# Kernel tuning notes

Hardware: AMD Instinct MI355X
Metric: run time of the kernel (lower is better)

Reference implementation:

```python
import jax, jax.numpy as jnp
import numpy as np

N_EMBD = 512
Q_N_EMBD = 512
N_HEAD = 8
EPS = 1e-5


def _layernorm(x, w, b):
    mu = jnp.mean(x, axis=-1, keepdims=True)
    var = jnp.mean(jnp.square(x - mu), axis=-1, keepdims=True)
    return (x - mu) * jax.lax.rsqrt(var + EPS) * w + b


def setup_inputs() -> dict:
    key = jax.random.key(0)
    ks = jax.random.split(key, 16)
    B, C, H, W = 8, N_EMBD, 32, 32
    s = 1.0 / np.sqrt(N_EMBD)
    inp = {
        "q": jax.random.normal(ks[0], (B, Q_N_EMBD, H, W), jnp.float32),
        "kv": jax.random.normal(ks[1], (B, C, H, W), jnp.float32),
        "ln_kv_w": jnp.ones((N_EMBD,), jnp.float32),
        "ln_kv_b": jnp.zeros((N_EMBD,), jnp.float32),
        "ln_q_w": jnp.ones((Q_N_EMBD,), jnp.float32),
        "ln_q_b": jnp.zeros((Q_N_EMBD,), jnp.float32),
        "Wk": jax.random.normal(ks[2], (N_EMBD, N_EMBD), jnp.float32) * s,
        "bk": jnp.zeros((N_EMBD,), jnp.float32),
        "Wq": jax.random.normal(ks[3], (Q_N_EMBD, N_EMBD), jnp.float32) * s,
        "bq": jnp.zeros((N_EMBD,), jnp.float32),
        "Wv": jax.random.normal(ks[4], (N_EMBD, N_EMBD), jnp.float32) * s,
        "bv": jnp.zeros((N_EMBD,), jnp.float32),
        "Wp": jax.random.normal(ks[5], (N_EMBD, N_EMBD), jnp.float32) * s,
        "bp": jnp.zeros((N_EMBD,), jnp.float32),
    }
    return inp


def reference(q, kv, ln_kv_w, ln_kv_b, ln_q_w, ln_q_b,
              Wk, bk, Wq, bq, Wv, bv, Wp, bp):
    B, C, H, W = kv.shape
    c_q = q.shape[1]
    T = H * W
    hd = C // N_HEAD  # head dim

    # [B, C, H, W] -> [B, T, C] tokens
    kv_t = kv.reshape(B, C, T).transpose(0, 2, 1)
    q_t = q.reshape(B, c_q, T).transpose(0, 2, 1)

    kv_n = _layernorm(kv_t, ln_kv_w, ln_kv_b)
    q_n = _layernorm(q_t, ln_q_w, ln_q_b)

    # projections, split heads: [B, T, C] -> [B, H, T, hd]
    def heads(x):
        return x.reshape(B, T, N_HEAD, hd).transpose(0, 2, 1, 3)

    k = heads(kv_n @ Wk + bk)
    qh = heads(q_n @ Wq + bq)
    v = heads(kv_n @ Wv + bv)

    att = jnp.einsum('bhqd,bhkd->bhqk', qh, k) * (1.0 / np.sqrt(hd))
    att = jax.nn.softmax(att, axis=-1)
    y = jnp.einsum('bhqk,bhkd->bhqd', att, v)
    y = y.transpose(0, 2, 1, 3).reshape(B, T, C)
    y = y @ Wp + bp

    x = kv_t + y  # residual on (pre-LN) kv tokens
    return x.transpose(0, 2, 1).reshape(B, C, H, W)
```

## Files before the change

kernel.cpp:

```cpp
#include <hip/hip_runtime.h>
#include <stdint.h>

#define DI static __device__ __forceinline__

typedef __attribute__((ext_vector_type(8))) short bh8;
typedef __attribute__((ext_vector_type(4))) float f4;

DI short f2bf(float f) {
  unsigned u = __float_as_uint(f);
  u += 0x7fffu + ((u >> 16) & 1u);
  return (short)(u >> 16);
}

DI unsigned pkbf(float a, float b) {
  unsigned ua = __float_as_uint(a) + 0x8000u;
  unsigned ub = __float_as_uint(b) + 0x8000u;
  return __builtin_amdgcn_perm(ub, ua, 0x07060302u);
}

DI unsigned char f2fp8(float f) {
  return (unsigned char)(__builtin_amdgcn_cvt_pk_fp8_f32(f, f, 0, false) & 0xff);
}

DI void gll16(const void* g, void* l) {
  __builtin_amdgcn_global_load_lds(
      (const __attribute__((address_space(1))) unsigned int*)g,
      (__attribute__((address_space(3))) unsigned int*)l, 16, 0, 0);
}

DI f4 mfma16(bh8 a, bh8 b, f4 c) {
  return __builtin_amdgcn_mfma_f32_16x16x32_bf16(a, b, c, 0, 0, 0);
}

DI f4 mfma8(long a, long b, f4 c) {
  return __builtin_amdgcn_mfma_f32_16x16x32_fp8_fp8(a, b, c, 0, 0, 0);
}

DI bh8 ld8(const short* p) { return *(const bh8*)p; }

__global__ __launch_bounds__(256) void prep_k(
    const float* __restrict__ kv, const float* __restrict__ qi,
    const float* __restrict__ kw, const float* __restrict__ kbv,
    const float* __restrict__ qw, const float* __restrict__ qbv,
    const float* __restrict__ Wk, const float* __restrict__ Wq,
    const float* __restrict__ Wv, const float* __restrict__ Wp,
    short* __restrict__ kvn, short* __restrict__ qn,
    short* __restrict__ Wt)
{
  __shared__ char sm[16 * 516 * 4 + 128];
  int role = blockIdx.y;
  int bx = blockIdx.x;
  int tid = threadIdx.x;

  if (role < 4) {
    if (bx >= 256) return;
    float (*ts)[33] = (float(*)[33])sm;
    const float* w = (role == 0) ? Wk : (role == 1) ? Wq : (role == 2) ? Wv : Wp;
    short* o = Wt + ((size_t)role << 18);
    int c0 = (bx & 15) << 5, r0 = (bx >> 4) << 5;
    int tx = tid & 31, ty = tid >> 5;
#pragma unroll
    for (int k = 0; k < 32; k += 8)
      ts[ty + k][tx] = w[((size_t)(r0 + ty + k) << 9) + c0 + tx];
    __syncthreads();
#pragma unroll
    for (int k = 0; k < 32; k += 8)
      o[((size_t)(c0 + ty + k) << 9) + r0 + tx] = f2bf(ts[tx][ty + k]);
    return;
  }

  float (*xs)[516] = (float(*)[516])sm;
  float* smean = (float*)(sm + 16 * 516 * 4);
  float* srstd = smean + 16;
  int which = role - 4;
  const float* x = which ? qi : kv;
  const float* w = which ? qw : kw;
  const float* bb = which ? qbv : kbv;
  short* o = which ? qn : kvn;
  int b = bx >> 6;
  int t0 = (bx & 63) << 4;
  const float* xb = x + ((size_t)b << 19) + (size_t)t0;
#pragma unroll
  for (int k = 0; k < 8; k++) {
    int idx = (k << 8) + tid;
    int c = idx >> 2, tt = (idx & 3) << 2;
    float4 v = *(const float4*)(xb + ((size_t)c << 10) + tt);
    xs[tt + 0][c] = v.x; xs[tt + 1][c] = v.y;
    xs[tt + 2][c] = v.z; xs[tt + 3][c] = v.w;
  }
  __syncthreads();
  {
    int t = tid >> 4, cp = tid & 15;
    float s = 0.f, s2 = 0.f;
#pragma unroll
    for (int k = 0; k < 8; k++) {
      float4 v = *(const float4*)&xs[t][(cp << 2) + (k << 6)];
      s  += v.x + v.y + v.z + v.w;
      s2 += v.x * v.x + v.y * v.y + v.z * v.z + v.w * v.w;
    }
#pragma unroll
    for (int m = 1; m < 16; m <<= 1) {
      s  += __shfl_xor(s,  m);
      s2 += __shfl_xor(s2, m);
    }
    if (cp == 0) {
      float mean = s * (1.f / 512.f);
      float var  = s2 * (1.f / 512.f) - mean * mean;
      smean[t] = mean;
      srstd[t] = rsqrtf(var + 1e-5f);
    }
  }
  __syncthreads();
#pragma unroll
  for (int k = 0; k < 8; k++) {
    int idx = (k << 8) + tid;
    int t = idx >> 7, c = (idx & 127) << 2;
    float4 v = *(const float4*)&xs[t][c];
    float4 wv = *(const float4*)(w + c);
    float4 bv4 = *(const float4*)(bb + c);
    float mu = smean[t], rs = srstd[t];
    float r0 = (v.x - mu) * rs * wv.x + bv4.x;
    float r1 = (v.y - mu) * rs * wv.y + bv4.y;
    float r2 = (v.z - mu) * rs * wv.z + bv4.z;
    float r3 = (v.w - mu) * rs * wv.w + bv4.w;
    uint2 pk; pk.x = pkbf(r0, r1); pk.y = pkbf(r2, r3);
    *(uint2*)(o + (((size_t)(b << 10) + t0 + t) << 9) + c) = pk;
  }
}

__global__ __launch_bounds__(256, 3) void gemm_qkv_k(
    const short* __restrict__ kvn, const short* __restrict__ qn,
    const short* __restrict__ Wt,
    const float* __restrict__ bk, const float* __restrict__ bq,
    const float* __restrict__ bv,
    unsigned char* __restrict__ kb8, unsigned char* __restrict__ qb8,
    unsigned char* __restrict__ vb8)
{
  __shared__ short As[128 * 64];
  __shared__ short Bs[128 * 64];
  int z = blockIdx.z;
  const short* A; const short* Bt; const float* bias;
  int m0, n0;
  if (z == 0)      { A = kvn;            Bt = Wt;             bias = bk; }
  else if (z == 1) { A = qn;             Bt = Wt + (1 << 18); bias = bq; }
  else             { A = Wt + (2 << 18); Bt = kvn;            bias = bv; }
  if (z == 2) { m0 = blockIdx.y << 7; n0 = blockIdx.x << 7; }
  else        { m0 = blockIdx.x << 7; n0 = blockIdx.y << 7; }
  int tid = threadIdx.x;
  int lane = tid & 63, wid = tid >> 6;
  int r = lane & 15, g = lane >> 4;
  int wrow = (wid >> 1) << 6, wcol = (wid & 1) << 6;
  f4 acc[4][4];
#pragma unroll
  for (int i = 0; i < 4; i++)
#pragma unroll
    for (int j = 0; j < 4; j++) {
      acc[i][j][0] = 0.f; acc[i][j][1] = 0.f;
      acc[i][j][2] = 0.f; acc[i][j][3] = 0.f;
    }
  for (int k0 = 0; k0 < 512; k0 += 64) {
    __syncthreads();
#pragma unroll
    for (int it = 0; it < 4; it++) {
      int n = (it << 8) + tid;
      int row = n >> 3;
      int c = (n & 7) ^ (row & 7);
      gll16(A  + ((size_t)(m0 + row) << 9) + k0 + (c << 3), As + (n << 3));
      gll16(Bt + ((size_t)(n0 + row) << 9) + k0 + (c << 3), Bs + (n << 3));
    }
    __syncthreads();
    bh8 a[2][4], b[2][4];
#pragma unroll
    for (int ks = 0; ks < 2; ks++) {
#pragma unroll
      for (int i = 0; i < 4; i++) {
        int R = wrow + (i << 4) + r;
        a[ks][i] = ld8(As + (R << 6) + ((((ks << 2) + g) ^ (R & 7)) << 3));
      }
#pragma unroll
      for (int j = 0; j < 4; j++) {
        int R = wcol + (j << 4) + r;
        b[ks][j] = ld8(Bs + (R << 6) + ((((ks << 2) + g) ^ (R & 7)) << 3));
      }
    }
#pragma unroll
    for (int ks = 0; ks < 2; ks++)
#pragma unroll
      for (int i = 0; i < 4; i++)
#pragma unroll
        for (int j = 0; j < 4; j++)
          acc[i][j] = mfma16(a[ks][i], b[ks][j], acc[i][j]);
  }
#pragma unroll
  for (int i = 0; i < 4; i++) {
#pragma unroll
    for (int j = 0; j < 4; j++) {
      int mm = m0 + wrow + (i << 4) + (g << 2);
      int nn = n0 + wcol + (j << 4) + r;
      if (z == 0) {
        float bvv = bias[nn];
        int h = nn >> 6, d = nn & 63;
#pragma unroll
        for (int q = 0; q < 4; q++) {
          int m = mm + q;
          int bb = m >> 10, t = m & 1023;
          int c = t & 255;
          int p = ((c & 15) << 4) | (c >> 4);
          size_t base = ((size_t)((bb * 8 + h) * 4 + (t >> 8)) << 14);
          kb8[base + (p << 6) + (((d >> 3) ^ (p & 7)) << 3) + (d & 7)] =
              f2fp8(acc[i][j][q] + bvv);
        }
      } else if (z == 1) {
        float bvv = bias[nn];
        int h = nn >> 6, d = nn & 63;
#pragma unroll
        for (int q = 0; q < 4; q++) {
          int m = mm + q;
          int bb = m >> 10, t = m & 1023;
          qb8[((((size_t)(bb * 8 + h)) << 10) + t) * 64 + d] =
              f2fp8(acc[i][j][q] + bvv);
        }
      } else {
        int bb = nn >> 10, t = nn & 1023;
        int tb = (t & 255) >> 3;
#pragma unroll
        for (int q = 0; q < 4; q++) {
          int m = mm + q;
          int h = m >> 6, d = m & 63;
          size_t base = ((size_t)((bb * 8 + h) * 4 + (t >> 8)) << 14);
          vb8[base + (d << 8) + ((tb ^ (d & 31)) << 3) + (t & 7)] =
              f2fp8(acc[i][j][q] + bias[m]);
        }
      }
    }
  }
}

__global__ __launch_bounds__(256, 2) void gemm_proj_k(
    const short* __restrict__ A, const short* __restrict__ Bt,
    const float* __restrict__ bias, float* __restrict__ outp,
    const float* __restrict__ resid)
{
  __shared__ short As[64 * 64];
  __shared__ short Bs[128 * 64];
  int m0 = blockIdx.y << 6, n0 = blockIdx.x << 7;
  int tid = threadIdx.x;
  int lane = tid & 63, wid = tid >> 6;
  int r = lane & 15, g = lane >> 4;
  int wrow = (wid >> 1) << 5, wcol = (wid & 1) << 6;
  f4 acc[2][4];
#pragma unroll
  for (int i = 0; i < 2; i++)
#pragma unroll
    for (int j = 0; j < 4; j++) {
      acc[i][j][0] = 0.f; acc[i][j][1] = 0.f;
      acc[i][j][2] = 0.f; acc[i][j][3] = 0.f;
    }
  for (int k0 = 0; k0 < 512; k0 += 64) {
    __syncthreads();
#pragma unroll
    for (int it = 0; it < 2; it++) {
      int n = (it << 8) + tid;
      int row = n >> 3;
      int c = (n & 7) ^ (row & 7);
      gll16(A + ((size_t)(m0 + row) << 9) + k0 + (c << 3), As + (n << 3));
    }
#pragma unroll
    for (int it = 0; it < 4; it++) {
      int n = (it << 8) + tid;
      int row = n >> 3;
      int c = (n & 7) ^ (row & 7);
      gll16(Bt + ((size_t)(n0 + row) << 9) + k0 + (c << 3), Bs + (n << 3));
    }
    __syncthreads();
    bh8 a[2][2], b[2][4];
#pragma unroll
    for (int ks = 0; ks < 2; ks++) {
#pragma unroll
      for (int i = 0; i < 2; i++) {
        int R = wrow + (i << 4) + r;
        a[ks][i] = ld8(As + (R << 6) + ((((ks << 2) + g) ^ (R & 7)) << 3));
      }
#pragma unroll
      for (int j = 0; j < 4; j++) {
        int R = wcol + (j << 4) + r;
        b[ks][j] = ld8(Bs + (R << 6) + ((((ks << 2) + g) ^ (R & 7)) << 3));
      }
    }
#pragma unroll
    for (int ks = 0; ks < 2; ks++)
#pragma unroll
      for (int i = 0; i < 2; i++)
#pragma unroll
        for (int j = 0; j < 4; j++)
          acc[i][j] = mfma16(a[ks][i], b[ks][j], acc[i][j]);
  }
#pragma unroll
  for (int i = 0; i < 2; i++) {
#pragma unroll
    for (int j = 0; j < 4; j++) {
      int mm = m0 + wrow + (i << 4) + (g << 2);
      int nn = n0 + wcol + (j << 4) + r;
      int bb = nn >> 10, t = nn & 1023;
#pragma unroll
      for (int q = 0; q < 4; q++) {
        int m = mm + q;
        size_t ad = ((((size_t)bb << 9) + m) << 10) + t;
        outp[ad] = acc[i][j][q] + bias[m] + resid[ad];
      }
    }
  }
}

__global__ __launch_bounds__(256, 2) void attn_k(
    const unsigned char* __restrict__ qb8, const unsigned char* __restrict__ kb8,
    const unsigned char* __restrict__ vb8, short* __restrict__ yo)
{
  __shared__ char Ks[16384];
  __shared__ char Vs[16384];
  __shared__ char Ps[32768];
  int h = blockIdx.x, b = blockIdx.z;
  int qt0 = blockIdx.y << 7;
  int tid = threadIdx.x, lane = tid & 63, wid = tid >> 6;
  int r = lane & 15, g = lane >> 4;
  int wbase = wid << 5;
  size_t bh = (size_t)(b * 8 + h);
  const unsigned char* Qg = qb8 + ((bh << 10) + qt0) * 64;
  const unsigned char* Kg = kb8 + (bh << 16);
  const unsigned char* Vg = vb8 + (bh << 16);

  long qf8[2][2];
#pragma unroll
  for (int i = 0; i < 2; i++)
#pragma unroll
    for (int ksd = 0; ksd < 2; ksd++)
      qf8[i][ksd] = *(const long*)(Qg +
          ((size_t)(wbase + (i << 4) + r) << 6) + (((ksd << 2) + g) << 3));

  const long ONES = 0x3838383838383838L;

  f4 oac[2][4], sacc[2];
#pragma unroll
  for (int i = 0; i < 2; i++) {
#pragma unroll
    for (int jn = 0; jn < 4; jn++) {
      oac[i][jn][0] = 0.f; oac[i][jn][1] = 0.f;
      oac[i][jn][2] = 0.f; oac[i][jn][3] = 0.f;
    }
    sacc[i][0] = 0.f; sacc[i][1] = 0.f; sacc[i][2] = 0.f; sacc[i][3] = 0.f;
  }

  const float csc = 0.18033688011112042f;

  for (int ck = 0; ck < 4; ck++) {
    __syncthreads();
#pragma unroll
    for (int it = 0; it < 4; it++) {
      int n = ((it << 8) + tid) << 4;
      gll16(Kg + (ck << 14) + n, Ks + n);
      gll16(Vg + (ck << 14) + n, Vs + n);
    }
    __syncthreads();

    long kf[2][16];
    f4 s[16];
#pragma unroll
    for (int i = 0; i < 2; i++) {
#pragma unroll
      for (int j = 0; j < 16; j++) {
        s[j][0] = 0.f; s[j][1] = 0.f; s[j][2] = 0.f; s[j][3] = 0.f;
      }
#pragma unroll
      for (int ksd = 0; ksd < 2; ksd++)
#pragma unroll
        for (int j = 0; j < 16; j++) {
          if (i == 0)
            kf[ksd][j] = *(const long*)(Ks + (((j << 4) + r) << 6) +
                            ((((ksd << 2) + g) ^ (r & 7)) << 3));
          s[j] = mfma8(qf8[i][ksd], kf[ksd][j], s[j]);
        }
#pragma unroll
      for (int q = 0; q < 4; q++) {
        float e[16];
#pragma unroll
        for (int j = 0; j < 16; j++)
          e[j] = __builtin_amdgcn_exp2f(
                     fminf(fmaf(s[j][q], csc, -3.0f), 8.5f));
        int w0 = 0, w1 = 0, w2 = 0, w3 = 0;
        w0 = __builtin_amdgcn_cvt_pk_fp8_f32(e[0],  e[1],  w0, false);
        w0 = __builtin_amdgcn_cvt_pk_fp8_f32(e[2],  e[3],  w0, true);
        w1 = __builtin_amdgcn_cvt_pk_fp8_f32(e[4],  e[5],  w1, false);
        w1 = __builtin_amdgcn_cvt_pk_fp8_f32(e[6],  e[7],  w1, true);
        w2 = __builtin_amdgcn_cvt_pk_fp8_f32(e[8],  e[9],  w2, false);
        w2 = __builtin_amdgcn_cvt_pk_fp8_f32(e[10], e[11], w2, true);
        w3 = __builtin_amdgcn_cvt_pk_fp8_f32(e[12], e[13], w3, false);
        w3 = __builtin_amdgcn_cvt_pk_fp8_f32(e[14], e[15], w3, true);
        long plo = ((long)(unsigned)w0) | ((long)w1 << 32);
        long phi = ((long)(unsigned)w2) | ((long)w3 << 32);
        int row = wbase + (i << 4) + (g << 2) + q;
        int cc = r ^ (row & 15);
        *(long*)(Ps + (row << 8) + (cc << 4))     = plo;
        *(long*)(Ps + (row << 8) + (cc << 4) + 8) = phi;
      }
    }

#pragma unroll
    for (int ks = 0; ks < 8; ks++) {
      long ap[2];
#pragma unroll
      for (int i = 0; i < 2; i++) {
        int row = wbase + (i << 4) + r;
        int cc = ((ks << 1) + (g >> 1)) ^ (row & 15);
        ap[i] = *(const long*)(Ps + (row << 8) + (cc << 4) + ((g & 1) << 3));
        sacc[i] = mfma8(ap[i], ONES, sacc[i]);
      }
#pragma unroll
      for (int jn = 0; jn < 4; jn++) {
        int d = (jn << 4) + r;
        long bv8 = *(const long*)(Vs + (d << 8) +
                      ((((ks << 2) + g) ^ (d & 31)) << 3));
#pragma unroll
        for (int i = 0; i < 2; i++)
          oac[i][jn] = mfma8(ap[i], bv8, oac[i][jn]);
      }
    }
  }

#pragma unroll
  for (int i = 0; i < 2; i++)
#pragma unroll
    for (int q = 0; q < 4; q++) {
      float inv = 1.f / (sacc[i][q] + 1e-20f);
      int trow = qt0 + wbase + (i << 4) + (g << 2) + q;
      size_t base = (((size_t)(b << 10) + trow) << 9) + (h << 6);
#pragma unroll
      for (int jn = 0; jn < 4; jn++)
        yo[base + (jn << 4) + r] = f2bf(oac[i][jn][q] * inv);
    }
}

extern "C" void kernel_launch(void* const* d_in, const int* in_sizes, int n_in,
                              void* d_out, int out_size, void* d_ws, size_t ws_size,
                              hipStream_t stream)
{
  const float* q    = (const float*)d_in[0];
  const float* kv   = (const float*)d_in[1];
  const float* lnkw = (const float*)d_in[2];
  const float* lnkb = (const float*)d_in[3];
  const float* lnqw = (const float*)d_in[4];
  const float* lnqb = (const float*)d_in[5];
  const float* Wk   = (const float*)d_in[6];
  const float* bk   = (const float*)d_in[7];
  const float* Wq   = (const float*)d_in[8];
  const float* bq   = (const float*)d_in[9];
  const float* Wv   = (const float*)d_in[10];
  const float* bv   = (const float*)d_in[11];
  const float* Wp   = (const float*)d_in[12];
  const float* bp   = (const float*)d_in[13];

  char* ws = (char*)d_ws;
  const size_t SZ = (size_t)8192 * 512 * 2;
  short* buf0 = (short*)(ws);
  short* qn   = (short*)(ws + SZ);
  unsigned char* kb8 = (unsigned char*)(ws + 2 * SZ);
  unsigned char* qb8 = (unsigned char*)(ws + 3 * SZ);
  unsigned char* vb8 = (unsigned char*)(ws + 4 * SZ);
  short* Wt   = (short*)(ws + 5 * SZ);
  if (ws_size < 5 * SZ + 4 * 512 * 512 * 2) return;

  prep_k<<<dim3(512, 6), 256, 0, stream>>>(kv, q, lnkw, lnkb, lnqw, lnqb,
                                           Wk, Wq, Wv, Wp, buf0, qn, Wt);
  gemm_qkv_k<<<dim3(64, 4, 3), 256, 0, stream>>>(buf0, qn, Wt, bk, bq, bv,
                                                 kb8, qb8, vb8);
  attn_k<<<dim3(8, 8, 8), 256, 0, stream>>>(qb8, kb8, vb8, buf0);
  gemm_proj_k<<<dim3(64, 8), 256, 0, stream>>>(Wt + (3 << 18), buf0, bp,
                                               (float*)d_out, kv);
}
```

Measured before the change: 169.8 us.

## Read K/V fragments directly from global memory and fold softmax scale into Q

The attention kernel no longer stages K and V chunks through shared memory. Each wave loads its MFMA operands straight from global memory, so the two barriers per chunk are gone and the LDS footprint shrinks. The projection kernel now writes K and V in plain, unswizzled layouts to match those direct loads. It also multiplies Q by the softmax scale before the fp8 conversion, so the exp step drops its fused multiply-add and -3 offset. In exchange, K/V reuse across waves now depends on L1/L2 caching rather than LDS. The narrower exp clamp, with no offset, and the scaled fp8 Q slightly change numerics.

```diff
diff --git a/kernel.cpp b/kernel.cpp
--- a/kernel.cpp
+++ b/kernel.cpp
@@ -191,6 +191,7 @@
         for (int j = 0; j < 4; j++)
           acc[i][j] = mfma16(a[ks][i], b[ks][j], acc[i][j]);
   }
+  const float csc = 0.18033688011112042f;
 #pragma unroll
   for (int i = 0; i < 4; i++) {
 #pragma unroll
@@ -207,8 +208,7 @@
           int c = t & 255;
           int p = ((c & 15) << 4) | (c >> 4);
           size_t base = ((size_t)((bb * 8 + h) * 4 + (t >> 8)) << 14);
-          kb8[base + (p << 6) + (((d >> 3) ^ (p & 7)) << 3) + (d & 7)] =
-              f2fp8(acc[i][j][q] + bvv);
+          kb8[base + (p << 6) + d] = f2fp8(acc[i][j][q] + bvv);
         }
       } else if (z == 1) {
         float bvv = bias[nn];
@@ -218,17 +218,15 @@
           int m = mm + q;
           int bb = m >> 10, t = m & 1023;
           qb8[((((size_t)(bb * 8 + h)) << 10) + t) * 64 + d] =
-              f2fp8(acc[i][j][q] + bvv);
+              f2fp8((acc[i][j][q] + bvv) * csc);
         }
       } else {
         int bb = nn >> 10, t = nn & 1023;
-        int tb = (t & 255) >> 3;
 #pragma unroll
         for (int q = 0; q < 4; q++) {
           int m = mm + q;
           int h = m >> 6, d = m & 63;
-          size_t base = ((size_t)((bb * 8 + h) * 4 + (t >> 8)) << 14);
-          vb8[base + (d << 8) + ((tb ^ (d & 31)) << 3) + (t & 7)] =
+          vb8[((size_t)(bb * 8 + h) << 16) + (d << 10) + t] =
               f2fp8(acc[i][j][q] + bias[m]);
         }
       }
@@ -316,8 +314,6 @@
     const unsigned char* __restrict__ qb8, const unsigned char* __restrict__ kb8,
     const unsigned char* __restrict__ vb8, short* __restrict__ yo)
 {
-  __shared__ char Ks[16384];
-  __shared__ char Vs[16384];
   __shared__ char Ps[32768];
   int h = blockIdx.x, b = blockIdx.z;
   int qt0 = blockIdx.y << 7;
@@ -350,18 +346,7 @@
     sacc[i][0] = 0.f; sacc[i][1] = 0.f; sacc[i][2] = 0.f; sacc[i][3] = 0.f;
   }
 
-  const float csc = 0.18033688011112042f;
-
   for (int ck = 0; ck < 4; ck++) {
-    __syncthreads();
-#pragma unroll
-    for (int it = 0; it < 4; it++) {
-      int n = ((it << 8) + tid) << 4;
-      gll16(Kg + (ck << 14) + n, Ks + n);
-      gll16(Vg + (ck << 14) + n, Vs + n);
-    }
-    __syncthreads();
-
     long kf[2][16];
     f4 s[16];
 #pragma unroll
@@ -375,8 +360,8 @@
 #pragma unroll
         for (int j = 0; j < 16; j++) {
           if (i == 0)
-            kf[ksd][j] = *(const long*)(Ks + (((j << 4) + r) << 6) +
-                            ((((ksd << 2) + g) ^ (r & 7)) << 3));
+            kf[ksd][j] = *(const long*)(Kg + (ck << 14) +
+                            (((j << 4) + r) << 6) + (((ksd << 2) + g) << 3));
           s[j] = mfma8(qf8[i][ksd], kf[ksd][j], s[j]);
         }
 #pragma unroll
@@ -384,8 +369,7 @@
         float e[16];
 #pragma unroll
         for (int j = 0; j < 16; j++)
-          e[j] = __builtin_amdgcn_exp2f(
-                     fminf(fmaf(s[j][q], csc, -3.0f), 8.5f));
+          e[j] = __builtin_amdgcn_exp2f(fminf(s[j][q], 8.5f));
         int w0 = 0, w1 = 0, w2 = 0, w3 = 0;
         w0 = __builtin_amdgcn_cvt_pk_fp8_f32(e[0],  e[1],  w0, false);
         w0 = __builtin_amdgcn_cvt_pk_fp8_f32(e[2],  e[3],  w0, true);
@@ -416,9 +400,8 @@
       }
 #pragma unroll
       for (int jn = 0; jn < 4; jn++) {
-        int d = (jn << 4) + r;
-        long bv8 = *(const long*)(Vs + (d << 8) +
-                      ((((ks << 2) + g) ^ (d & 31)) << 3));
+        long bv8 = *(const long*)(Vg + (((size_t)((jn << 4) + r)) << 10) +
+                                  (ck << 8) + (ks << 5) + (g << 3));
 #pragma unroll
         for (int i = 0; i < 2; i++)
           oac[i][jn] = mfma8(ap[i], bv8, oac[i][jn]);
```

Measured after the change: 190.7 us. 12.3% more time.
